# Kernel optimization log

Hardware: AMD Instinct MI355X
Metric: run time of the kernel (lower is better)

Reference implementation:

```python
import jax, jax.numpy as jnp
from jax import lax
import numpy as np

B, S, E, HID = 16, 7, 64, 64
RES = (64, 64); D = RES[0] * RES[1]
XLOW, XHIGH = -0.5, 0.5
RLOW, RHIGH = float(np.sqrt(0.01)), float(np.sqrt(0.05))
PIXEL_MULT = 1.0; N_ITER = 3; TSOFT = 1.0 / float(np.sqrt(E))

def _build_grid():
    ranges = [np.linspace(XLOW, XHIGH, r) for r in RES]
    g = np.stack(np.meshgrid(*ranges, indexing='xy'), axis=-1)
    g = g.reshape(RES[0], RES[1], -1).reshape(1, -1, 2)
    return jnp.asarray(g, dtype=jnp.float32)

ABS_GRID = _build_grid()  # [1, D, 2]

def _ln(x, g, b):
    m = jnp.mean(x, -1, keepdims=True)
    v = jnp.mean(jnp.square(x - m), -1, keepdims=True)
    return (x - m) * lax.rsqrt(v + 1e-5) * g + b

def _forward(data, slot_noise, pos_rand, conv0_w, conv0_b, conv1_w, conv1_b, conv2_w, conv2_b,
             dataN_g, dataN_b, queryN_g, queryN_b, toK_w, toK_b, toV_w, toV_b, dense_w, dense_b,
             mlp1_w, mlp1_b, mlp2_w, mlp2_b, gru_wih, gru_whh, gru_bih, gru_bhh,
             alpha1_w, alpha1_b, alpha2_w, alpha2_b, final1_w, final1_b, final2_w, final2_b,
             slots_mu, slots_logsigma):
    dn = ('NCHW', 'OIHW', 'NCHW')
    def conv(x, w, b):
        return lax.conv_general_dilated(x, w, (1, 1), 'SAME', dimension_numbers=dn) + b[None, :, None, None]
    # CNN encoder: Conv-ReLU x3, 'same' padding, k=5
    x = jax.nn.relu(conv(data, conv0_w, conv0_b))
    x = jax.nn.relu(conv(x, conv1_w, conv1_b))
    x = jax.nn.relu(conv(x, conv2_w, conv2_b))
    enc = x.transpose(0, 2, 3, 1).reshape(B, D, HID)
    enc = _ln(enc, dataN_g, dataN_b)

    queries = slots_mu + jnp.exp(slots_logsigma) * slot_noise  # [B,S,E]
    # init_slots: faithful replication (source indexes the SLOT dim, and swaps rlow/rhigh)
    pos_scale = pos_rand.at[:, :2, :].add(-0.5)
    pos_scale = pos_scale.at[:, -1, :].set((RLOW - RHIGH) * pos_rand[:, -1, :] + RHIGH)

    encK = enc @ toK_w + toK_b  # [B,D,E]
    encV = enc @ toV_w + toV_b

    def init_mlp(y):
        y = _ln(y, queryN_g, queryN_b)
        return jax.nn.relu(y @ mlp1_w + mlp1_b) @ mlp2_w + mlp2_b

    def get_kv(ps):
        # per-slot relative grid: [B,S,D,2]
        rel = (ABS_GRID[:, None] - ps[:, :, None, :2]) / ps[:, :, -1][:, :, None, None]
        eg = PIXEL_MULT * (rel @ dense_w + dense_b)  # [B,S,D,E]
        return init_mlp(encK[:, None] + eg), init_mlp(encV[:, None] + eg)

    def att_wts(q, k):
        logits = jnp.einsum('bse,bsde->bsd', q, k) * TSOFT
        att = jax.nn.softmax(logits, axis=1)  # softmax over slots
        wts = att / jnp.sum(att, -1, keepdims=True) + 1e-8
        return att, wts

    def update_frames(wts):
        new_pos = jnp.einsum('bsd,de->bse', wts, ABS_GRID[0])  # [B,S,2]
        d2 = jnp.sum(jnp.square(ABS_GRID[:, None] - new_pos[:, :, None]), -1)  # [B,S,D]
        new_scale = jnp.sqrt(jnp.einsum('bsd,bsd->bs', wts, d2))
        return jnp.concatenate([new_pos, new_scale[..., None]], -1)

    def gru(xg, h):
        gi = xg @ gru_wih.T + gru_bih
        gh = h @ gru_whh.T + gru_bhh
        ir, iz, inn = jnp.split(gi, 3, -1)
        hr, hz, hn = jnp.split(gh, 3, -1)
        r = jax.nn.sigmoid(ir + hr)
        z = jax.nn.sigmoid(iz + hz)
        n = jnp.tanh(inn + r * hn)
        return (1.0 - z) * n + z * h

    for _ in range(N_ITER):
        keys, vals = get_kv(pos_scale)
        att, wts = att_wts(_ln(queries, queryN_g, queryN_b), keys)
        pos_scale = update_frames(wts)
        upd = jnp.einsum('bsd,bsde->bse', wts, vals)
        queries = gru(upd.reshape(-1, E), queries.reshape(-1, E)).reshape(B, S, E)

    keys, _ = get_kv(pos_scale)
    att, wts = att_wts(_ln(queries, queryN_g, queryN_b), keys)
    nps = update_frames(wts)
    alpha = jax.nn.sigmoid(jax.nn.relu(queries @ alpha1_w + alpha1_b) @ alpha2_w + alpha2_b)
    slot_feat = jax.nn.relu(queries @ final1_w + final1_b) @ final2_w + final2_b + nps
    return queries, att, slot_feat, alpha

def setup_inputs() -> dict:
    ks = jax.random.split(jax.random.key(0), 20)
    f32 = jnp.float32
    def rn(i, shape, s):
        return jax.random.normal(ks[i], shape, f32) * s
    inp = dict(
        data=jax.random.normal(ks[0], (B, 1, RES[0], RES[1]), f32),
        slot_noise=jax.random.normal(ks[1], (B, S, E), f32),
        pos_rand=jax.random.uniform(ks[2], (B, S, 3), dtype=f32),
        conv0_w=rn(3, (HID, 1, 5, 5), 0.2), conv0_b=jnp.zeros(HID, f32),
        conv1_w=rn(4, (HID, HID, 5, 5), 0.025), conv1_b=jnp.zeros(HID, f32),
        conv2_w=rn(5, (HID, HID, 5, 5), 0.025), conv2_b=jnp.zeros(HID, f32),
        dataN_g=jnp.ones(HID, f32), dataN_b=jnp.zeros(HID, f32),
        queryN_g=jnp.ones(E, f32), queryN_b=jnp.zeros(E, f32),
        toK_w=rn(6, (HID, E), 0.125), toK_b=jnp.zeros(E, f32),
        toV_w=rn(7, (HID, E), 0.125), toV_b=jnp.zeros(E, f32),
        dense_w=rn(8, (2, E), 0.7), dense_b=jnp.zeros(E, f32),
        mlp1_w=rn(9, (E, E), 0.125), mlp1_b=jnp.zeros(E, f32),
        mlp2_w=rn(10, (E, E), 0.125), mlp2_b=jnp.zeros(E, f32),
        gru_wih=rn(11, (3 * E, E), 0.125), gru_whh=rn(12, (3 * E, E), 0.125),
        gru_bih=jnp.zeros(3 * E, f32), gru_bhh=jnp.zeros(3 * E, f32),
        alpha1_w=rn(13, (E, 32), 0.125), alpha1_b=jnp.zeros(32, f32),
        alpha2_w=rn(14, (32, 1), 0.18), alpha2_b=jnp.zeros(1, f32),
        final1_w=rn(15, (E, HID), 0.125), final1_b=jnp.zeros(HID, f32),
        final2_w=rn(16, (HID, 3), 0.125), final2_b=jnp.zeros(3, f32),
        slots_mu=rn(17, (1, 1, E), 1.0),
        slots_logsigma=rn(18, (1, 1, E), 0.01),
    )
    return inp

def reference(data, slot_noise, pos_rand, conv0_w, conv0_b, conv1_w, conv1_b, conv2_w, conv2_b,
              dataN_g, dataN_b, queryN_g, queryN_b, toK_w, toK_b, toV_w, toV_b, dense_w, dense_b,
              mlp1_w, mlp1_b, mlp2_w, mlp2_b, gru_wih, gru_whh, gru_bih, gru_bhh,
              alpha1_w, alpha1_b, alpha2_w, alpha2_b, final1_w, final1_b, final2_w, final2_b,
              slots_mu, slots_logsigma):
    return _forward(data, slot_noise, pos_rand, conv0_w, conv0_b, conv1_w, conv1_b, conv2_w, conv2_b,
                    dataN_g, dataN_b, queryN_g, queryN_b, toK_w, toK_b, toV_w, toV_b, dense_w, dense_b,
                    mlp1_w, mlp1_b, mlp2_w, mlp2_b, gru_wih, gru_whh, gru_bih, gru_bhh,
                    alpha1_w, alpha1_b, alpha2_w, alpha2_b, final1_w, final1_b, final2_w, final2_b,
                    slots_mu, slots_logsigma)
```

## Files before the change

### kernel.cpp

```cpp
#include <hip/hip_runtime.h>
#include <cmath>


#define RLOW_F 0.1f
#define RHIGH_F 0.22360679774997896f

typedef __attribute__((ext_vector_type(8))) __bf16 bf16x8;
typedef __attribute__((ext_vector_type(4))) float f32x4;

__device__ __forceinline__ float wsum64(float v){
  #pragma unroll
  for (int off = 32; off > 0; off >>= 1) v += __shfl_xor(v, off, 64);
  return v;
}
__device__ __forceinline__ float rdlane(float v, int l){
  return __int_as_float(__builtin_amdgcn_readlane(__float_as_int(v), l));
}
__device__ __forceinline__ unsigned short bf16bits(float v){
  __bf16 h = (__bf16)v;
  return *reinterpret_cast<unsigned short*>(&h);
}

__global__ void k_prep(const float* __restrict__ noise, const float* __restrict__ prand,
                       const float* __restrict__ mu, const float* __restrict__ logsig,
                       float* __restrict__ queries, float* __restrict__ ps){
  int row = blockIdx.x;
  int e = threadIdx.x;
  int s = row % 7;
  queries[row*64 + e] = mu[e] + expf(logsig[e]) * noise[row*64 + e];
  if (e < 3){
    float pr = prand[row*3 + e];
    float v;
    if (s < 2)      v = pr - 0.5f;
    else if (s == 6) v = (RLOW_F - RHIGH_F)*pr + RHIGH_F;
    else            v = pr;
    ps[row*3 + e] = v;
  }
}

__global__ __launch_bounds__(256) void k_conv0(const float* __restrict__ in,
                        const float* __restrict__ w, const float* __restrict__ bias,
                        unsigned short* __restrict__ out){
  int bi = blockIdx.x; int b = bi >> 6; int y = bi & 63;
  int t = threadIdx.x; int lane = t & 63; int xg = t >> 6;
  __shared__ float s_in[5*68];
  __shared__ float s_w[64*25];
  __shared__ float s_out[64*65];
  for (int i = t; i < 1600; i += 256) s_w[i] = w[i];
  for (int i = t; i < 340; i += 256){
    int r = i / 68, cx = i % 68;
    int yy = y + r - 2, gx = cx - 2;
    float v = 0.f;
    if (yy >= 0 && yy < 64 && gx >= 0 && gx < 64) v = in[(b*64 + yy)*64 + gx];
    s_in[r*68 + cx] = v;
  }
  __syncthreads();
  int o = lane;
  float bv = bias[o];
  float acc[16];
  #pragma unroll
  for (int k = 0; k < 16; k++) acc[k] = bv;
  #pragma unroll
  for (int ky = 0; ky < 5; ky++){
    float rv[20];
    const float4* p = reinterpret_cast<const float4*>(&s_in[ky*68 + xg*16]);
    #pragma unroll
    for (int q = 0; q < 5; q++){ float4 f = p[q]; rv[q*4]=f.x; rv[q*4+1]=f.y; rv[q*4+2]=f.z; rv[q*4+3]=f.w; }
    #pragma unroll
    for (int kx = 0; kx < 5; kx++){
      float wv = s_w[o*25 + ky*5 + kx];
      #pragma unroll
      for (int k = 0; k < 16; k++) acc[k] = fmaf(rv[k+kx], wv, acc[k]);
    }
  }
  #pragma unroll
  for (int k = 0; k < 16; k++) s_out[o*65 + xg*16 + k] = fmaxf(acc[k], 0.f);
  __syncthreads();
  for (int i = t; i < 4096; i += 256){
    int px = i >> 6, ch = i & 63;
    out[((size_t)(b*64 + y)*64 + px)*64 + ch] = bf16bits(s_out[ch*65 + px]);
  }
}

__global__ void k_packconv(const float* __restrict__ w, unsigned short* __restrict__ out){
  int idx = blockIdx.x*256 + threadIdx.x;
  if (idx >= 102400) return;
  int j = idx & 7;
  int l = (idx >> 3) & 63;
  int frag = idx >> 9;
  int nt = frag & 3;
  int ks = (frag >> 2) % 10;
  int dy = frag / 40;
  int q = l >> 4, cr = l & 15;
  int k = ks*32 + q*8 + j;
  int kx = k >> 6, ch = k & 63;
  int n = nt*16 + cr;
  out[idx] = bf16bits(w[((n*64 + ch)*5 + dy)*5 + kx]);
}

__global__ __launch_bounds__(256) void k_convm(const unsigned short* __restrict__ in_bf,
                        const unsigned short* __restrict__ wpack,
                        const float* __restrict__ bias,
                        const float* __restrict__ lng, const float* __restrict__ lnb,
                        unsigned short* __restrict__ out_bf, float* __restrict__ out_f,
                        int mode){
  int bi = blockIdx.x;
  int b = bi >> 4; int yg = bi & 15;
  int t = threadIdx.x; int wv = t >> 6; int l = t & 63;
  int q = l >> 4, cr = l & 15;
  int p0 = wv*16;

  __shared__ char lds[8*68*144];

  for (int ri = 0; ri < 8; ri++){
    int yy = yg*4 + ri - 2;
    bool rok = (yy >= 0 && yy < 64);
    const uint4* src = reinterpret_cast<const uint4*>(in_bf + (size_t)(b*64 + yy)*64*64);
    for (int i = t; i < 544; i += 256){
      int px = i >> 3, c8 = i & 7;
      uint4 v = {0u,0u,0u,0u};
      int gx = px - 2;
      if (rok && gx >= 0 && gx < 64) v = src[gx*8 + c8];
      *reinterpret_cast<uint4*>(&lds[ri*9792 + px*144 + c8*16]) = v;
    }
  }
  __syncthreads();

  f32x4 acc[4][4];
  #pragma unroll
  for (int r = 0; r < 4; r++)
    #pragma unroll
    for (int nt = 0; nt < 4; nt++) acc[r][nt] = (f32x4){0.f,0.f,0.f,0.f};

  const bf16x8* wp = reinterpret_cast<const bf16x8*>(wpack);
  for (int dy = 0; dy < 5; dy++){
    for (int ks = 0; ks < 10; ks++){
      bf16x8 Bf[4];
      int fbase = (dy*10 + ks)*4;
      #pragma unroll
      for (int nt = 0; nt < 4; nt++) Bf[nt] = wp[(fbase + nt)*64 + l];
      int aoff = (p0 + cr + (ks >> 1))*144 + (ks & 1)*64 + q*16;
      #pragma unroll
      for (int r = 0; r < 4; r++){
        bf16x8 a = *reinterpret_cast<const bf16x8*>(&lds[(r + dy)*9792 + aoff]);
        #pragma unroll
        for (int nt = 0; nt < 4; nt++)
          acc[r][nt] = __builtin_amdgcn_mfma_f32_16x16x32_bf16(a, Bf[nt], acc[r][nt], 0, 0, 0);
      }
    }
  }

  float bv[4];
  #pragma unroll
  for (int nt = 0; nt < 4; nt++) bv[nt] = bias[nt*16 + cr];

  if (mode == 0){
    #pragma unroll
    for (int r = 0; r < 4; r++){
      int y = yg*4 + r;
      #pragma unroll
      for (int reg = 0; reg < 4; reg++){
        int p = p0 + q*4 + reg;
        size_t base = ((size_t)(b*64 + y)*64 + p)*64;
        #pragma unroll
        for (int nt = 0; nt < 4; nt++)
          out_bf[base + nt*16 + cr] = bf16bits(fmaxf(acc[r][nt][reg] + bv[nt], 0.f));
      }
    }
  } else {
    float gv[4], bb[4];
    #pragma unroll
    for (int nt = 0; nt < 4; nt++){ gv[nt] = lng[nt*16 + cr]; bb[nt] = lnb[nt*16 + cr]; }
    #pragma unroll
    for (int r = 0; r < 4; r++){
      int y = yg*4 + r;
      #pragma unroll
      for (int reg = 0; reg < 4; reg++){
        int p = p0 + q*4 + reg;
        float v[4]; float s1 = 0.f, s2 = 0.f;
        #pragma unroll
        for (int nt = 0; nt < 4; nt++){
          v[nt] = fmaxf(acc[r][nt][reg] + bv[nt], 0.f);
          s1 += v[nt]; s2 += v[nt]*v[nt];
        }
        #pragma unroll
        for (int m = 1; m < 16; m <<= 1){ s1 += __shfl_xor(s1, m, 64); s2 += __shfl_xor(s2, m, 64); }
        float mean = s1 * (1.f/64.f);
        float var  = s2 * (1.f/64.f) - mean*mean;
        float rstd = 1.0f/sqrtf(var + 1e-5f);
        size_t base = ((size_t)b*4096 + y*64 + p)*64;
        #pragma unroll
        for (int nt = 0; nt < 4; nt++)
          out_f[base + nt*16 + cr] = (v[nt] - mean)*rstd*gv[nt] + bb[nt];
      }
    }
  }
}

__global__ void k_packw1(const float* __restrict__ w1, unsigned short* __restrict__ out){
  int idx = blockIdx.x*256 + threadIdx.x;
  int jj = idx & 7;
  int lane = (idx >> 3) & 63;
  int frag = idx >> 9;
  int ks = frag >> 2, nt = frag & 3;
  int q = lane >> 4, cr = lane & 15;
  int k = ks*32 + q*8 + jj;
  int n = nt*16 + cr;
  out[idx] = bf16bits(w1[k*64 + n]);
}

__global__ __launch_bounds__(256) void k_projm(const float* __restrict__ enc,
                       const unsigned short* __restrict__ kpack, const float* __restrict__ bk,
                       const unsigned short* __restrict__ vpack, const float* __restrict__ bvp,
                       float* __restrict__ K, float* __restrict__ V){
  int bi = blockIdx.x; int b = bi >> 6; int tile = bi & 63;
  int t = threadIdx.x; int wv = t >> 6; int l = t & 63;
  int q = l >> 4, cr = l & 15;
  int d0 = tile*64 + wv*16;

  const bf16x8* kp = reinterpret_cast<const bf16x8*>(kpack);
  const bf16x8* vp = reinterpret_cast<const bf16x8*>(vpack);
  bf16x8 KB[8], VB[8];
  #pragma unroll
  for (int f = 0; f < 8; f++){ KB[f] = kp[f*64 + l]; VB[f] = vp[f*64 + l]; }

  const float* er = enc + (size_t)(b*4096 + d0 + cr)*64;
  bf16x8 a0, a1;
  #pragma unroll
  for (int h = 0; h < 2; h++){
    const float4* e4 = reinterpret_cast<const float4*>(er + (h ? (32 + q*8) : (q*8)));
    #pragma unroll
    for (int p = 0; p < 2; p++){
      float4 e = e4[p];
      if (h == 0){ a0[p*4+0]=(__bf16)e.x; a0[p*4+1]=(__bf16)e.y; a0[p*4+2]=(__bf16)e.z; a0[p*4+3]=(__bf16)e.w; }
      else       { a1[p*4+0]=(__bf16)e.x; a1[p*4+1]=(__bf16)e.y; a1[p*4+2]=(__bf16)e.z; a1[p*4+3]=(__bf16)e.w; }
    }
  }

  f32x4 zero = {0.f,0.f,0.f,0.f};
  f32x4 aK[4], aV[4];
  #pragma unroll
  for (int nt = 0; nt < 4; nt++){
    aK[nt] = __builtin_amdgcn_mfma_f32_16x16x32_bf16(a0, KB[nt],     zero,   0, 0, 0);
    aK[nt] = __builtin_amdgcn_mfma_f32_16x16x32_bf16(a1, KB[4 + nt], aK[nt], 0, 0, 0);
    aV[nt] = __builtin_amdgcn_mfma_f32_16x16x32_bf16(a0, VB[nt],     zero,   0, 0, 0);
    aV[nt] = __builtin_amdgcn_mfma_f32_16x16x32_bf16(a1, VB[4 + nt], aV[nt], 0, 0, 0);
  }
  #pragma unroll
  for (int nt = 0; nt < 4; nt++){
    float bkv = bk[nt*16 + cr], bvv = bvp[nt*16 + cr];
    #pragma unroll
    for (int reg = 0; reg < 4; reg++){
      size_t base = ((size_t)b*4096 + d0 + q*4 + reg)*64 + nt*16 + cr;
      K[base] = aK[nt][reg] + bkv;
      V[base] = aV[nt][reg] + bvv;
    }
  }
}

__global__ void k_phaseprep(const float* __restrict__ queries, const float* __restrict__ ps,
                            const float* __restrict__ qg_, const float* __restrict__ qb_,
                            const float* __restrict__ dw, const float* __restrict__ db,
                            const float* __restrict__ mlp2w, const float* __restrict__ mlp2b,
                            float* __restrict__ absc, float* __restrict__ w2qc,
                            float* __restrict__ sum_att, float* __restrict__ upd){
  int row = blockIdx.x; int e = threadIdx.x;
  float q = queries[row*64 + e];
  float m = wsum64(q) * (1.f/64.f);
  float d = q - m;
  float var = wsum64(d*d) * (1.f/64.f);
  float qlnv = d * (1.0f/sqrtf(var + 1e-5f)) * qg_[e] + qb_[e];
  float px = ps[row*3], py = ps[row*3+1], sc = ps[row*3+2];
  float A  = dw[e]      / sc;
  float Bv = dw[64 + e] / sc;
  absc[(row*3+0)*64 + e] = A;
  absc[(row*3+1)*64 + e] = Bv;
  absc[(row*3+2)*64 + e] = db[e] - px*A - py*Bv;
  float acc = 0.f;
  const float* wrow = mlp2w + e*64;
  for (int j = 0; j < 64; j++) acc = fmaf(wrow[j], rdlane(qlnv, j), acc);
  w2qc[row*68 + e] = acc;
  float c2 = wsum64(mlp2b[e] * qlnv);
  if (e == 0) w2qc[row*68 + 64] = c2;
  upd[row*64 + e] = 0.f;
  if (e == 0) sum_att[row] = 0.f;
}

__global__ __launch_bounds__(256) void k_attn(const float* __restrict__ encX,
     const unsigned short* __restrict__ w1pack, const float* __restrict__ mlp1b,
     const float* __restrict__ absc, const float* __restrict__ qg_,
     const float* __restrict__ qb_, const float* __restrict__ w2qc,
     const float* __restrict__ att, const float* __restrict__ sum_att,
     float* __restrict__ outp, int mode){
  int t = threadIdx.x; int wv = t >> 6; int l = t & 63;
  int q = l >> 4, cr = l & 15;
  int bs = blockIdx.x >> 6; int tile = blockIdx.x & 63;
  int b = bs / 7;
  int m0 = tile*64 + wv*16;
  int drow = m0 + cr;

  const bf16x8* wp = reinterpret_cast<const bf16x8*>(w1pack);
  bf16x8 Bf[8];
  #pragma unroll
  for (int f = 0; f < 8; f++) Bf[f] = wp[f*64 + l];

  const float* Ac = absc + bs*192;
  const float* er = encX + (size_t)(b*4096 + drow)*64;
  float gx = -0.5f + (float)(drow & 63) * (1.f/63.f);
  float gy = -0.5f + (float)((drow >> 6) & 63) * (1.f/63.f);
  float x[16];
  #pragma unroll
  for (int h = 0; h < 2; h++){
    int fb = h ? (32 + q*8) : (q*8);
    const float4* e4 = reinterpret_cast<const float4*>(er + fb);
    const float4* A4 = reinterpret_cast<const float4*>(Ac + fb);
    const float4* B4 = reinterpret_cast<const float4*>(Ac + 64 + fb);
    const float4* C4 = reinterpret_cast<const float4*>(Ac + 128 + fb);
    #pragma unroll
    for (int p = 0; p < 2; p++){
      float4 e = e4[p], Av = A4[p], Bv = B4[p], Cv = C4[p];
      int o = h*8 + p*4;
      x[o+0] = e.x + gx*Av.x + gy*Bv.x + Cv.x;
      x[o+1] = e.y + gx*Av.y + gy*Bv.y + Cv.y;
      x[o+2] = e.z + gx*Av.z + gy*Bv.z + Cv.z;
      x[o+3] = e.w + gx*Av.w + gy*Bv.w + Cv.w;
    }
  }
  float s = 0.f;
  #pragma unroll
  for (int k = 0; k < 16; k++) s += x[k];
  s += __shfl_xor(s, 16, 64); s += __shfl_xor(s, 32, 64);
  float m = s * (1.f/64.f);
  float v = 0.f;
  #pragma unroll
  for (int k = 0; k < 16; k++){ float dd = x[k] - m; v += dd*dd; }
  v += __shfl_xor(v, 16, 64); v += __shfl_xor(v, 32, 64);
  float rstd = 1.0f/sqrtf(v * (1.f/64.f) + 1e-5f);

  bf16x8 a0, a1;
  #pragma unroll
  for (int h = 0; h < 2; h++){
    int fb = h ? (32 + q*8) : (q*8);
    const float4* g4 = reinterpret_cast<const float4*>(qg_ + fb);
    const float4* b4 = reinterpret_cast<const float4*>(qb_ + fb);
    #pragma unroll
    for (int p = 0; p < 2; p++){
      float4 gg = g4[p], bb = b4[p];
      int o = h*8 + p*4;
      float r0 = (x[o+0]-m)*rstd*gg.x + bb.x;
      float r1 = (x[o+1]-m)*rstd*gg.y + bb.y;
      float r2 = (x[o+2]-m)*rstd*gg.z + bb.z;
      float r3 = (x[o+3]-m)*rstd*gg.w + bb.w;
      if (h == 0){ a0[p*4+0]=(__bf16)r0; a0[p*4+1]=(__bf16)r1; a0[p*4+2]=(__bf16)r2; a0[p*4+3]=(__bf16)r3; }
      else       { a1[p*4+0]=(__bf16)r0; a1[p*4+1]=(__bf16)r1; a1[p*4+2]=(__bf16)r2; a1[p*4+3]=(__bf16)r3; }
    }
  }

  f32x4 zero = {0.f, 0.f, 0.f, 0.f};
  f32x4 acc[4];
  #pragma unroll
  for (int nt = 0; nt < 4; nt++){
    acc[nt] = __builtin_amdgcn_mfma_f32_16x16x32_bf16(a0, Bf[nt],     zero,    0, 0, 0);
    acc[nt] = __builtin_amdgcn_mfma_f32_16x16x32_bf16(a1, Bf[4 + nt], acc[nt], 0, 0, 0);
  }

  if (mode == 0){
    const float* wq = w2qc + bs*68;
    float c2 = wq[64];
    float p[4] = {0.f, 0.f, 0.f, 0.f};
    #pragma unroll
    for (int nt = 0; nt < 4; nt++){
      float bb  = mlp1b[nt*16 + cr];
      float wqv = wq[nt*16 + cr];
      #pragma unroll
      for (int reg = 0; reg < 4; reg++){
        float y = fmaxf(acc[nt][reg] + bb, 0.f);
        p[reg] = fmaf(y, wqv, p[reg]);
      }
    }
    #pragma unroll
    for (int reg = 0; reg < 4; reg++){
      #pragma unroll
      for (int off = 1; off < 16; off <<= 1) p[reg] += __shfl_xor(p[reg], off, 64);
    }
    if (cr == 0){
      #pragma unroll
      for (int reg = 0; reg < 4; reg++)
        outp[bs*4096 + m0 + q*4 + reg] = (p[reg] + c2) * 0.125f;
    }
  } else {
    float sa = sum_att[bs];
    float wr[4];
    #pragma unroll
    for (int reg = 0; reg < 4; reg++)
      wr[reg] = att[bs*4096 + m0 + q*4 + reg] / sa + 1e-8f;
    float pc[4] = {0.f, 0.f, 0.f, 0.f};
    #pragma unroll
    for (int nt = 0; nt < 4; nt++){
      float bb = mlp1b[nt*16 + cr];
      #pragma unroll
      for (int reg = 0; reg < 4; reg++)
        pc[nt] = fmaf(wr[reg], fmaxf(acc[nt][reg] + bb, 0.f), pc[nt]);
    }
    #pragma unroll
    for (int nt = 0; nt < 4; nt++){
      pc[nt] += __shfl_xor(pc[nt], 16, 64);
      pc[nt] += __shfl_xor(pc[nt], 32, 64);
    }
    __shared__ float red[4][64];
    if (q == 0){
      #pragma unroll
      for (int nt = 0; nt < 4; nt++) red[wv][nt*16 + cr] = pc[nt];
    }
    __syncthreads();
    if (t < 64) atomicAdd(&outp[bs*64 + t], red[0][t] + red[1][t] + red[2][t] + red[3][t]);
  }
}

__global__ void k_softmax(float* __restrict__ att, float* __restrict__ sum_att){
  int bi = blockIdx.x;
  int b = bi >> 4;
  int t = threadIdx.x;
  int d = (bi & 15)*256 + t;
  int lane = t & 63; int w = t >> 6;
  __shared__ float red[4];
  float l[7];
  #pragma unroll
  for (int s = 0; s < 7; s++) l[s] = att[(b*7+s)*4096 + d];
  float m = l[0];
  #pragma unroll
  for (int s = 1; s < 7; s++) m = fmaxf(m, l[s]);
  float sum = 0.f;
  #pragma unroll
  for (int s = 0; s < 7; s++){ l[s] = expf(l[s] - m); sum += l[s]; }
  for (int s = 0; s < 7; s++){
    float a = l[s] / sum;
    att[(b*7+s)*4096 + d] = a;
    float ws = wsum64(a);
    if (lane == 0) red[w] = ws;
    __syncthreads();
    if (t == 0) atomicAdd(&sum_att[b*7+s], red[0]+red[1]+red[2]+red[3]);
    __syncthreads();
  }
}

__global__ void k_frames(const float* __restrict__ att, const float* __restrict__ sum_att,
                         float* __restrict__ psout, float* __restrict__ sumw){
  int bs = blockIdx.x; int t = threadIdx.x;
  float sa = sum_att[bs];
  float a0 = 0.f, ax = 0.f, ay = 0.f, a2 = 0.f;
  for (int d = t; d < 4096; d += 256){
    float wv = att[bs*4096 + d] / sa + 1e-8f;
    float gx = -0.5f + (float)(d & 63) * (1.f/63.f);
    float gy = -0.5f + (float)(d >> 6) * (1.f/63.f);
    a0 += wv; ax += wv*gx; ay += wv*gy; a2 += wv*(gx*gx + gy*gy);
  }
  __shared__ float red[4][4];
  int lane = t & 63, w = t >> 6;
  a0 = wsum64(a0); ax = wsum64(ax); ay = wsum64(ay); a2 = wsum64(a2);
  if (lane == 0){ red[w][0]=a0; red[w][1]=ax; red[w][2]=ay; red[w][3]=a2; }
  __syncthreads();
  if (t == 0){
    float W0=0,Wx=0,Wy=0,Wg=0;
    for (int k = 0; k < 4; k++){ W0+=red[k][0]; Wx+=red[k][1]; Wy+=red[k][2]; Wg+=red[k][3]; }
    float s2 = Wg - (Wx*Wx + Wy*Wy)*(2.f - W0);
    psout[bs*3+0] = Wx; psout[bs*3+1] = Wy; psout[bs*3+2] = sqrtf(fmaxf(s2, 0.f));
    sumw[bs] = W0;
  }
}

__global__ void k_gru(const float* __restrict__ upd, float* __restrict__ queries,
                      const float* __restrict__ wih, const float* __restrict__ whh,
                      const float* __restrict__ bih, const float* __restrict__ bhh,
                      const float* __restrict__ mlp2w, const float* __restrict__ mlp2b,
                      const float* __restrict__ sumw){
  int row = blockIdx.x; int t = threadIdx.x;
  __shared__ float us[64], hs[64], xs[64], gis[192], ghs[192];
  if (t < 64){ us[t] = upd[row*64 + t]; hs[t] = queries[row*64 + t]; }
  __syncthreads();
  if (t < 64){
    float a = sumw[row] * mlp2b[t];
    for (int i = 0; i < 64; i++) a = fmaf(us[i], mlp2w[i*64 + t], a);
    xs[t] = a;
  }
  __syncthreads();
  float gi = bih[t], gh = bhh[t];
  for (int e = 0; e < 64; e++){
    gi = fmaf(wih[t*64 + e], xs[e], gi);
    gh = fmaf(whh[t*64 + e], hs[e], gh);
  }
  gis[t] = gi; ghs[t] = gh;
  __syncthreads();
  if (t < 64){
    float r = 1.0f/(1.0f + expf(-(gis[t]      + ghs[t])));
    float z = 1.0f/(1.0f + expf(-(gis[64+t]   + ghs[64+t])));
    float n = tanhf(gis[128+t] + r*ghs[128+t]);
    queries[row*64 + t] = (1.0f - z)*n + z*hs[t];
  }
}

__global__ void k_final(const float* __restrict__ queries, const float* __restrict__ nps,
                        const float* __restrict__ a1w, const float* __restrict__ a1b,
                        const float* __restrict__ a2w, const float* __restrict__ a2b,
                        const float* __restrict__ f1w, const float* __restrict__ f1b,
                        const float* __restrict__ f2w, const float* __restrict__ f2b,
                        float* __restrict__ out){
  int bs = blockIdx.x; int e = threadIdx.x;
  __shared__ float qs[64], hf[64], ha[32];
  float q = queries[bs*64 + e];
  qs[e] = q;
  out[bs*64 + e] = q;
  __syncthreads();
  float accf = f1b[e];
  for (int i = 0; i < 64; i++) accf = fmaf(qs[i], f1w[i*64 + e], accf);
  hf[e] = fmaxf(accf, 0.f);
  if (e < 32){
    float acca = a1b[e];
    for (int i = 0; i < 64; i++) acca = fmaf(qs[i], a1w[i*32 + e], acca);
    ha[e] = fmaxf(acca, 0.f);
  }
  __syncthreads();
  if (e < 3){
    float sf = f2b[e];
    for (int o = 0; o < 64; o++) sf = fmaf(hf[o], f2w[o*3 + e], sf);
    out[465920 + bs*3 + e] = sf + nps[bs*3 + e];
  }
  if (e == 32){
    float al = a2b[0];
    for (int o = 0; o < 32; o++) al = fmaf(ha[o], a2w[o], al);
    out[466256 + bs] = 1.0f/(1.0f + expf(-al));
  }
}

extern "C" void kernel_launch(void* const* d_in, const int* in_sizes, int n_in,
                              void* d_out, int out_size, void* d_ws, size_t ws_size,
                              hipStream_t stream){
  const float* data        = (const float*)d_in[0];
  const float* slot_noise  = (const float*)d_in[1];
  const float* pos_rand    = (const float*)d_in[2];
  const float* conv0_w     = (const float*)d_in[3];
  const float* conv0_b     = (const float*)d_in[4];
  const float* conv1_w     = (const float*)d_in[5];
  const float* conv1_b     = (const float*)d_in[6];
  const float* conv2_w     = (const float*)d_in[7];
  const float* conv2_b     = (const float*)d_in[8];
  const float* dataN_g     = (const float*)d_in[9];
  const float* dataN_b     = (const float*)d_in[10];
  const float* queryN_g    = (const float*)d_in[11];
  const float* queryN_b    = (const float*)d_in[12];
  const float* toK_w       = (const float*)d_in[13];
  const float* toK_b       = (const float*)d_in[14];
  const float* toV_w       = (const float*)d_in[15];
  const float* toV_b       = (const float*)d_in[16];
  const float* dense_w     = (const float*)d_in[17];
  const float* dense_b     = (const float*)d_in[18];
  const float* mlp1_w      = (const float*)d_in[19];
  const float* mlp1_b      = (const float*)d_in[20];
  const float* mlp2_w      = (const float*)d_in[21];
  const float* mlp2_b      = (const float*)d_in[22];
  const float* gru_wih     = (const float*)d_in[23];
  const float* gru_whh     = (const float*)d_in[24];
  const float* gru_bih     = (const float*)d_in[25];
  const float* gru_bhh     = (const float*)d_in[26];
  const float* alpha1_w    = (const float*)d_in[27];
  const float* alpha1_b    = (const float*)d_in[28];
  const float* alpha2_w    = (const float*)d_in[29];
  const float* alpha2_b    = (const float*)d_in[30];
  const float* final1_w    = (const float*)d_in[31];
  const float* final1_b    = (const float*)d_in[32];
  const float* final2_w    = (const float*)d_in[33];
  const float* final2_b    = (const float*)d_in[34];
  const float* slots_mu    = (const float*)d_in[35];
  const float* slots_lsig  = (const float*)d_in[36];

  float* ws   = (float*)d_ws;
  float* bufA = ws;
  float* bufB = bufA + 4194304;
  float* bufC = bufB + 4194304;
  float* attw = bufC + 4194304;
  float* queries = attw + 458752;
  float* ps   = queries + 7168;
  float* absc = ps + 512;
  float* sum_att = absc + 21504;
  float* upd  = sum_att + 128;
  float* nps  = upd + 7168;
  float* w2qc = nps + 512;
  float* sumw = w2qc + 7616;
  unsigned short* w1pack = (unsigned short*)(sumw + 128);
  unsigned short* kpack  = w1pack + 4096;
  unsigned short* vpack  = kpack + 4096;
  unsigned short* wp1    = vpack + 4096;
  unsigned short* wp2    = wp1 + 102400;

  unsigned short* c0_bf = (unsigned short*)bufA;
  unsigned short* c1_bf = (unsigned short*)bufC;
  float* enc  = bufB;
  float* encK = bufA;
  float* encV = bufC;

  float* outq   = (float*)d_out;
  float* outatt = outq + 7168;

  k_prep<<<112, 64, 0, stream>>>(slot_noise, pos_rand, slots_mu, slots_lsig, queries, ps);
  k_packw1<<<16, 256, 0, stream>>>(mlp1_w, w1pack);
  k_packw1<<<16, 256, 0, stream>>>(toK_w, kpack);
  k_packw1<<<16, 256, 0, stream>>>(toV_w, vpack);
  k_packconv<<<400, 256, 0, stream>>>(conv1_w, wp1);
  k_packconv<<<400, 256, 0, stream>>>(conv2_w, wp2);
  k_conv0<<<1024, 256, 0, stream>>>(data, conv0_w, conv0_b, c0_bf);
  k_convm<<<256, 256, 0, stream>>>(c0_bf, wp1, conv1_b, nullptr, nullptr, c1_bf, nullptr, 0);
  k_convm<<<256, 256, 0, stream>>>(c1_bf, wp2, conv2_b, dataN_g, dataN_b, nullptr, enc, 1);
  k_projm<<<1024, 256, 0, stream>>>(enc, kpack, toK_b, vpack, toV_b, encK, encV);

  for (int p = 0; p < 4; p++){
    float* attp = (p == 3) ? outatt : attw;
    k_phaseprep<<<112, 64, 0, stream>>>(queries, ps, queryN_g, queryN_b, dense_w, dense_b,
                                        mlp2_w, mlp2_b, absc, w2qc, sum_att, upd);
    k_attn<<<7168, 256, 0, stream>>>(encK, w1pack, mlp1_b, absc, queryN_g, queryN_b,
                                     w2qc, attp, sum_att, attp, 0);
    k_softmax<<<256, 256, 0, stream>>>(attp, sum_att);
    k_frames<<<112, 256, 0, stream>>>(attp, sum_att, (p == 3) ? nps : ps, sumw);
    if (p < 3){
      k_attn<<<7168, 256, 0, stream>>>(encV, w1pack, mlp1_b, absc, queryN_g, queryN_b,
                                       w2qc, attp, sum_att, upd, 1);
      k_gru<<<112, 192, 0, stream>>>(upd, queries, gru_wih, gru_whh, gru_bih, gru_bhh,
                                     mlp2_w, mlp2_b, sumw);
    }
  }
  k_final<<<112, 64, 0, stream>>>(queries, nps, alpha1_w, alpha1_b, alpha2_w, alpha2_b,
                                  final1_w, final1_b, final2_w, final2_b, outq);
}
```

Baseline: 595.7 us.

## Fold query LayerNorm and MLP1 into precomputed per-pixel key/value projections

The change expands the per-slot LayerNorm plus MLP1 algebraically. The LN-weighted mlp1 matrix is folded into the K/V projections, producing bf16 UK/UV tensors and per-pixel statistics (sum, sum of squares, dot products with the dense weights). Each phase then runs a single attention kernel per batch tile covering all 7 slots, accumulating frame moments and updates with atomics. This replaces the separate phaseprep, per-slot attention, softmax and frames kernels. The aim is to cut the repeated 64x64 MFMA work and launch count per phase, at the cost of atomic contention, changed precision (bf16 intermediates, variance via expanded moments) and hardcoding the weight-sum constant.

Measured after the change: 607.4 us. Within noise of the previous version (+2.0%).

```diff
diff --git a/kernel.cpp b/kernel.cpp
--- a/kernel.cpp
+++ b/kernel.cpp
@@ -4,6 +4,7 @@
 
 #define RLOW_F 0.1f
 #define RHIGH_F 0.22360679774997896f
+#define W0CONST 1.00004096f
 
 typedef __attribute__((ext_vector_type(8))) __bf16 bf16x8;
 typedef __attribute__((ext_vector_type(4))) float f32x4;
@@ -20,21 +21,122 @@
   __bf16 h = (__bf16)v;
   return *reinterpret_cast<unsigned short*>(&h);
 }
+__device__ __forceinline__ float bf16val(unsigned short u){
+  __bf16 h = *reinterpret_cast<__bf16*>(&u);
+  return (float)h;
+}
+
+__device__ __forceinline__ void pp_core(int row, int e, float qv,
+    const float* __restrict__ qg_, const float* __restrict__ qb_,
+    const float* __restrict__ mlp2w, const float* __restrict__ mlp2b,
+    float* __restrict__ w2qc){
+  float m = wsum64(qv) * (1.f/64.f);
+  float d = qv - m;
+  float var = wsum64(d*d) * (1.f/64.f);
+  float qlnv = d * (1.0f/sqrtf(var + 1e-5f)) * qg_[e] + qb_[e];
+  float acc = 0.f;
+  const float* wrow = mlp2w + e*64;
+  for (int j = 0; j < 64; j++) acc = fmaf(wrow[j], rdlane(qlnv, j), acc);
+  w2qc[row*68 + e] = acc;
+  float c2 = wsum64(mlp2b[e] * qlnv);
+  if (e == 0) w2qc[row*68 + 64] = c2;
+}
 
 __global__ void k_prep(const float* __restrict__ noise, const float* __restrict__ prand,
                        const float* __restrict__ mu, const float* __restrict__ logsig,
-                       float* __restrict__ queries, float* __restrict__ ps){
+                       const float* __restrict__ qg_, const float* __restrict__ qb_,
+                       const float* __restrict__ mlp2w, const float* __restrict__ mlp2b,
+                       float* __restrict__ queries, float* __restrict__ ps,
+                       float* __restrict__ w2qc, float* __restrict__ accF,
+                       float* __restrict__ gp1, float* __restrict__ gp2){
   int row = blockIdx.x;
   int e = threadIdx.x;
   int s = row % 7;
-  queries[row*64 + e] = mu[e] + expf(logsig[e]) * noise[row*64 + e];
+  float qv = mu[e] + expf(logsig[e]) * noise[row*64 + e];
+  queries[row*64 + e] = qv;
+  gp1[row*64 + e] = 0.f;
+  gp2[row*64 + e] = 0.f;
+  if (e < 4) accF[row*4 + e] = 0.f;
   if (e < 3){
     float pr = prand[row*3 + e];
-    float v;
-    if (s < 2)      v = pr - 0.5f;
-    else if (s == 6) v = (RLOW_F - RHIGH_F)*pr + RHIGH_F;
-    else            v = pr;
-    ps[row*3 + e] = v;
+    float pv;
+    if (s < 2)       pv = pr - 0.5f;
+    else if (s == 6) pv = (RLOW_F - RHIGH_F)*pr + RHIGH_F;
+    else             pv = pr;
+    ps[row*3 + e] = pv;
+  }
+  pp_core(row, e, qv, qg_, qb_, mlp2w, mlp2b, w2qc);
+}
+
+__global__ void k_wconsts(const float* __restrict__ w1, const float* __restrict__ b1,
+                          const float* __restrict__ qg, const float* __restrict__ qb,
+                          const float* __restrict__ dw, const float* __restrict__ db,
+                          const float* __restrict__ tokw, const float* __restrict__ tovw,
+                          const float* __restrict__ bk, const float* __restrict__ bv,
+                          float* __restrict__ consts,
+                          unsigned short* __restrict__ wckp, unsigned short* __restrict__ wcvp){
+  __shared__ float wck[4096], wcv[4096];
+  int t = threadIdx.x;
+  for (int i = 0; i < 16; i++){
+    int idx = t*16 + i; int k = idx >> 6, n = idx & 63;
+    float a1 = 0.f, a2 = 0.f;
+    for (int j = 0; j < 64; j++){
+      float w = qg[j]*w1[j*64 + n];
+      a1 = fmaf(tokw[k*64 + j], w, a1);
+      a2 = fmaf(tovw[k*64 + j], w, a2);
+    }
+    wck[idx] = a1; wcv[idx] = a2;
+  }
+  if (t < 64){
+    int n = t;
+    float G=0,P0=0,Q0=0,Rb=0,Zq=0,bK=0,bV=0;
+    for (int k = 0; k < 64; k++){
+      float w = w1[k*64 + n];
+      float wg = qg[k]*w;
+      G += wg;
+      P0 = fmaf(dw[k],    wg, P0);
+      Q0 = fmaf(dw[64+k], wg, Q0);
+      Rb = fmaf(db[k],    wg, Rb);
+      Zq = fmaf(qb[k],    w,  Zq);
+      bK = fmaf(bk[k],    wg, bK);
+      bV = fmaf(bv[k],    wg, bV);
+    }
+    consts[n] = G; consts[64+n] = P0; consts[128+n] = Q0;
+    consts[192+n] = Zq + b1[n];
+    consts[256+n] = bK + Rb; consts[320+n] = bV + Rb;
+  }
+  if (t >= 64 && t < 73){
+    int j = t - 64; float s = 0.f;
+    for (int k = 0; k < 64; k++){
+      float a, bq;
+      switch(j){
+        case 0: a=dw[k];    bq=dw[k];    break;
+        case 1: a=dw[64+k]; bq=dw[64+k]; break;
+        case 2: a=db[k];    bq=db[k];    break;
+        case 3: a=dw[k];    bq=dw[64+k]; break;
+        case 4: a=dw[k];    bq=db[k];    break;
+        case 5: a=dw[64+k]; bq=db[k];    break;
+        case 6: a=dw[k];    bq=1.f;      break;
+        case 7: a=dw[64+k]; bq=1.f;      break;
+        default:a=db[k];    bq=1.f;      break;
+      }
+      s = fmaf(a, bq, s);
+    }
+    consts[384 + j] = s;
+  }
+  if (t == 73){
+    float s = 0.f;
+    for (int i = 0; i < 64; i++){ float c = -0.5f + i*(1.f/63.f); s += c*c; }
+    consts[393] = 128.f * s;
+  }
+  __syncthreads();
+  for (int i = 0; i < 16; i++){
+    int o = t*16 + i;
+    int jj = o & 7, lane = (o >> 3) & 63, frag = o >> 9;
+    int ks = frag >> 2, nt = frag & 3, qq = lane >> 4, cc = lane & 15;
+    int k = ks*32 + qq*8 + jj, n = nt*16 + cc;
+    wckp[o] = bf16bits(wck[k*64 + n]);
+    wcvp[o] = bf16bits(wcv[k*64 + n]);
   }
 }
 
@@ -56,10 +158,10 @@
   }
   __syncthreads();
   int o = lane;
-  float bv = bias[o];
+  float bvv = bias[o];
   float acc[16];
   #pragma unroll
-  for (int k = 0; k < 16; k++) acc[k] = bv;
+  for (int k = 0; k < 16; k++) acc[k] = bvv;
   #pragma unroll
   for (int ky = 0; ky < 5; ky++){
     float rv[20];
@@ -150,9 +252,9 @@
     }
   }
 
-  float bv[4];
-  #pragma unroll
-  for (int nt = 0; nt < 4; nt++) bv[nt] = bias[nt*16 + cr];
+  float bvv[4];
+  #pragma unroll
+  for (int nt = 0; nt < 4; nt++) bvv[nt] = bias[nt*16 + cr];
 
   if (mode == 0){
     #pragma unroll
@@ -164,7 +266,7 @@
         size_t base = ((size_t)(b*64 + y)*64 + p)*64;
         #pragma unroll
         for (int nt = 0; nt < 4; nt++)
-          out_bf[base + nt*16 + cr] = bf16bits(fmaxf(acc[r][nt][reg] + bv[nt], 0.f));
+          out_bf[base + nt*16 + cr] = bf16bits(fmaxf(acc[r][nt][reg] + bvv[nt], 0.f));
       }
     }
   } else {
@@ -180,7 +282,7 @@
         float v[4]; float s1 = 0.f, s2 = 0.f;
         #pragma unroll
         for (int nt = 0; nt < 4; nt++){
-          v[nt] = fmaxf(acc[r][nt][reg] + bv[nt], 0.f);
+          v[nt] = fmaxf(acc[r][nt][reg] + bvv[nt], 0.f);
           s1 += v[nt]; s2 += v[nt]*v[nt];
         }
         #pragma unroll
@@ -210,20 +312,18 @@
 }
 
 __global__ __launch_bounds__(256) void k_projm(const float* __restrict__ enc,
-                       const unsigned short* __restrict__ kpack, const float* __restrict__ bk,
-                       const unsigned short* __restrict__ vpack, const float* __restrict__ bvp,
-                       float* __restrict__ K, float* __restrict__ V){
+      const unsigned short* __restrict__ kpack, const float* __restrict__ bk,
+      const unsigned short* __restrict__ vpack, const float* __restrict__ bv,
+      const unsigned short* __restrict__ wckp, const unsigned short* __restrict__ wcvp,
+      const float* __restrict__ consts, const float* __restrict__ dw,
+      const float* __restrict__ db,
+      unsigned short* __restrict__ UK, unsigned short* __restrict__ UV,
+      float* __restrict__ stats){
   int bi = blockIdx.x; int b = bi >> 6; int tile = bi & 63;
   int t = threadIdx.x; int wv = t >> 6; int l = t & 63;
   int q = l >> 4, cr = l & 15;
   int d0 = tile*64 + wv*16;
 
-  const bf16x8* kp = reinterpret_cast<const bf16x8*>(kpack);
-  const bf16x8* vp = reinterpret_cast<const bf16x8*>(vpack);
-  bf16x8 KB[8], VB[8];
-  #pragma unroll
-  for (int f = 0; f < 8; f++){ KB[f] = kp[f*64 + l]; VB[f] = vp[f*64 + l]; }
-
   const float* er = enc + (size_t)(b*4096 + d0 + cr)*64;
   bf16x8 a0, a1;
   #pragma unroll
@@ -238,248 +338,275 @@
   }
 
   f32x4 zero = {0.f,0.f,0.f,0.f};
-  f32x4 aK[4], aV[4];
+  f32x4 aK[4], aV[4], aUK[4], aUV[4];
+  {
+    const bf16x8* kp = reinterpret_cast<const bf16x8*>(kpack);
+    const bf16x8* vp = reinterpret_cast<const bf16x8*>(vpack);
+    #pragma unroll
+    for (int nt = 0; nt < 4; nt++){
+      bf16x8 k0 = kp[nt*64 + l], k1 = kp[(4+nt)*64 + l];
+      bf16x8 v0 = vp[nt*64 + l], v1 = vp[(4+nt)*64 + l];
+      aK[nt] = __builtin_amdgcn_mfma_f32_16x16x32_bf16(a0, k0, zero,   0, 0, 0);
+      aK[nt] = __builtin_amdgcn_mfma_f32_16x16x32_bf16(a1, k1, aK[nt], 0, 0, 0);
+      aV[nt] = __builtin_amdgcn_mfma_f32_16x16x32_bf16(a0, v0, zero,   0, 0, 0);
+      aV[nt] = __builtin_amdgcn_mfma_f32_16x16x32_bf16(a1, v1, aV[nt], 0, 0, 0);
+    }
+  }
+  {
+    const bf16x8* cp = reinterpret_cast<const bf16x8*>(wckp);
+    const bf16x8* dp = reinterpret_cast<const bf16x8*>(wcvp);
+    #pragma unroll
+    for (int nt = 0; nt < 4; nt++){
+      bf16x8 c0 = cp[nt*64 + l], c1 = cp[(4+nt)*64 + l];
+      bf16x8 e0 = dp[nt*64 + l], e1 = dp[(4+nt)*64 + l];
+      aUK[nt] = __builtin_amdgcn_mfma_f32_16x16x32_bf16(a0, c0, zero,    0, 0, 0);
+      aUK[nt] = __builtin_amdgcn_mfma_f32_16x16x32_bf16(a1, c1, aUK[nt], 0, 0, 0);
+      aUV[nt] = __builtin_amdgcn_mfma_f32_16x16x32_bf16(a0, e0, zero,    0, 0, 0);
+      aUV[nt] = __builtin_amdgcn_mfma_f32_16x16x32_bf16(a1, e1, aUV[nt], 0, 0, 0);
+    }
+  }
+
+  float bKn[4], bVn[4], uKn[4], uVn[4], d0n[4], d1n[4], dbn[4];
   #pragma unroll
   for (int nt = 0; nt < 4; nt++){
-    aK[nt] = __builtin_amdgcn_mfma_f32_16x16x32_bf16(a0, KB[nt],     zero,   0, 0, 0);
-    aK[nt] = __builtin_amdgcn_mfma_f32_16x16x32_bf16(a1, KB[4 + nt], aK[nt], 0, 0, 0);
-    aV[nt] = __builtin_amdgcn_mfma_f32_16x16x32_bf16(a0, VB[nt],     zero,   0, 0, 0);
-    aV[nt] = __builtin_amdgcn_mfma_f32_16x16x32_bf16(a1, VB[4 + nt], aV[nt], 0, 0, 0);
-  }
-  #pragma unroll
-  for (int nt = 0; nt < 4; nt++){
-    float bkv = bk[nt*16 + cr], bvv = bvp[nt*16 + cr];
+    int n = nt*16 + cr;
+    bKn[nt] = bk[n]; bVn[nt] = bv[n];
+    uKn[nt] = consts[256 + n]; uVn[nt] = consts[320 + n];
+    d0n[nt] = dw[n]; d1n[nt] = dw[64 + n]; dbn[nt] = db[n];
+  }
+
+  float T[10][4];
+  #pragma unroll
+  for (int j = 0; j < 10; j++)
+    #pragma unroll
+    for (int r = 0; r < 4; r++) T[j][r] = 0.f;
+
+  #pragma unroll
+  for (int reg = 0; reg < 4; reg++){
+    int d = d0 + q*4 + reg;
+    size_t base = (size_t)(b*4096 + d)*64;
+    #pragma unroll
+    for (int nt = 0; nt < 4; nt++){
+      int n = nt*16 + cr;
+      UK[base + n] = bf16bits(aUK[nt][reg] + uKn[nt]);
+      UV[base + n] = bf16bits(aUV[nt][reg] + uVn[nt]);
+      float eK = aK[nt][reg] + bKn[nt];
+      float eV = aV[nt][reg] + bVn[nt];
+      T[0][reg] += eK;           T[5][reg] += eV;
+      T[1][reg] += eK*eK;        T[6][reg] += eV*eV;
+      T[2][reg] = fmaf(eK, d0n[nt], T[2][reg]);  T[7][reg] = fmaf(eV, d0n[nt], T[7][reg]);
+      T[3][reg] = fmaf(eK, d1n[nt], T[3][reg]);  T[8][reg] = fmaf(eV, d1n[nt], T[8][reg]);
+      T[4][reg] = fmaf(eK, dbn[nt], T[4][reg]);  T[9][reg] = fmaf(eV, dbn[nt], T[9][reg]);
+    }
+  }
+  #pragma unroll
+  for (int st = 0; st < 10; st++)
+    #pragma unroll
+    for (int r = 0; r < 4; r++){
+      #pragma unroll
+      for (int m = 1; m < 16; m <<= 1) T[st][r] += __shfl_xor(T[st][r], m, 64);
+    }
+  if (cr == 0){
     #pragma unroll
     for (int reg = 0; reg < 4; reg++){
-      size_t base = ((size_t)b*4096 + d0 + q*4 + reg)*64 + nt*16 + cr;
-      K[base] = aK[nt][reg] + bkv;
-      V[base] = aV[nt][reg] + bvv;
-    }
-  }
-}
-
-__global__ void k_phaseprep(const float* __restrict__ queries, const float* __restrict__ ps,
-                            const float* __restrict__ qg_, const float* __restrict__ qb_,
-                            const float* __restrict__ dw, const float* __restrict__ db,
-                            const float* __restrict__ mlp2w, const float* __restrict__ mlp2b,
-                            float* __restrict__ absc, float* __restrict__ w2qc,
-                            float* __restrict__ sum_att, float* __restrict__ upd){
-  int row = blockIdx.x; int e = threadIdx.x;
-  float q = queries[row*64 + e];
-  float m = wsum64(q) * (1.f/64.f);
-  float d = q - m;
-  float var = wsum64(d*d) * (1.f/64.f);
-  float qlnv = d * (1.0f/sqrtf(var + 1e-5f)) * qg_[e] + qb_[e];
-  float px = ps[row*3], py = ps[row*3+1], sc = ps[row*3+2];
-  float A  = dw[e]      / sc;
-  float Bv = dw[64 + e] / sc;
-  absc[(row*3+0)*64 + e] = A;
-  absc[(row*3+1)*64 + e] = Bv;
-  absc[(row*3+2)*64 + e] = db[e] - px*A - py*Bv;
-  float acc = 0.f;
-  const float* wrow = mlp2w + e*64;
-  for (int j = 0; j < 64; j++) acc = fmaf(wrow[j], rdlane(qlnv, j), acc);
-  w2qc[row*68 + e] = acc;
-  float c2 = wsum64(mlp2b[e] * qlnv);
-  if (e == 0) w2qc[row*68 + 64] = c2;
-  upd[row*64 + e] = 0.f;
-  if (e == 0) sum_att[row] = 0.f;
-}
-
-__global__ __launch_bounds__(256) void k_attn(const float* __restrict__ encX,
-     const unsigned short* __restrict__ w1pack, const float* __restrict__ mlp1b,
-     const float* __restrict__ absc, const float* __restrict__ qg_,
-     const float* __restrict__ qb_, const float* __restrict__ w2qc,
-     const float* __restrict__ att, const float* __restrict__ sum_att,
-     float* __restrict__ outp, int mode){
+      int d = d0 + q*4 + reg;
+      float* sp = stats + (size_t)(b*4096 + d)*12;
+      #pragma unroll
+      for (int j = 0; j < 10; j++) sp[j] = T[j][reg];
+    }
+  }
+}
+
+__global__ __launch_bounds__(256) void k_attn(
+    const unsigned short* __restrict__ UK, const unsigned short* __restrict__ UV,
+    const float* __restrict__ stats, const float* __restrict__ consts,
+    const float* __restrict__ ps, const float* __restrict__ w2qc,
+    float* __restrict__ accF, float* __restrict__ gp1, float* __restrict__ gp2,
+    float* __restrict__ att_out, int mode){
+  int bi = blockIdx.x;
+  int b = bi >> 6, tile = bi & 63;
   int t = threadIdx.x; int wv = t >> 6; int l = t & 63;
   int q = l >> 4, cr = l & 15;
-  int bs = blockIdx.x >> 6; int tile = blockIdx.x & 63;
-  int b = bs / 7;
-  int m0 = tile*64 + wv*16;
-  int drow = m0 + cr;
-
-  const bf16x8* wp = reinterpret_cast<const bf16x8*>(w1pack);
-  bf16x8 Bf[8];
-  #pragma unroll
-  for (int f = 0; f < 8; f++) Bf[f] = wp[f*64 + l];
-
-  const float* Ac = absc + bs*192;
-  const float* er = encX + (size_t)(b*4096 + drow)*64;
-  float gx = -0.5f + (float)(drow & 63) * (1.f/63.f);
-  float gy = -0.5f + (float)((drow >> 6) & 63) * (1.f/63.f);
-  float x[16];
-  #pragma unroll
-  for (int h = 0; h < 2; h++){
-    int fb = h ? (32 + q*8) : (q*8);
-    const float4* e4 = reinterpret_cast<const float4*>(er + fb);
-    const float4* A4 = reinterpret_cast<const float4*>(Ac + fb);
-    const float4* B4 = reinterpret_cast<const float4*>(Ac + 64 + fb);
-    const float4* C4 = reinterpret_cast<const float4*>(Ac + 128 + fb);
-    #pragma unroll
-    for (int p = 0; p < 2; p++){
-      float4 e = e4[p], Av = A4[p], Bv = B4[p], Cv = C4[p];
-      int o = h*8 + p*4;
-      x[o+0] = e.x + gx*Av.x + gy*Bv.x + Cv.x;
-      x[o+1] = e.y + gx*Av.y + gy*Bv.y + Cv.y;
-      x[o+2] = e.z + gx*Av.z + gy*Bv.z + Cv.z;
-      x[o+3] = e.w + gx*Av.w + gy*Bv.w + Cv.w;
-    }
-  }
-  float s = 0.f;
-  #pragma unroll
-  for (int k = 0; k < 16; k++) s += x[k];
-  s += __shfl_xor(s, 16, 64); s += __shfl_xor(s, 32, 64);
-  float m = s * (1.f/64.f);
-  float v = 0.f;
-  #pragma unroll
-  for (int k = 0; k < 16; k++){ float dd = x[k] - m; v += dd*dd; }
-  v += __shfl_xor(v, 16, 64); v += __shfl_xor(v, 32, 64);
-  float rstd = 1.0f/sqrtf(v * (1.f/64.f) + 1e-5f);
-
-  bf16x8 a0, a1;
-  #pragma unroll
-  for (int h = 0; h < 2; h++){
-    int fb = h ? (32 + q*8) : (q*8);
-    const float4* g4 = reinterpret_cast<const float4*>(qg_ + fb);
-    const float4* b4 = reinterpret_cast<const float4*>(qb_ + fb);
-    #pragma unroll
-    for (int p = 0; p < 2; p++){
-      float4 gg = g4[p], bb = b4[p];
-      int o = h*8 + p*4;
-      float r0 = (x[o+0]-m)*rstd*gg.x + bb.x;
-      float r1 = (x[o+1]-m)*rstd*gg.y + bb.y;
-      float r2 = (x[o+2]-m)*rstd*gg.z + bb.z;
-      float r3 = (x[o+3]-m)*rstd*gg.w + bb.w;
-      if (h == 0){ a0[p*4+0]=(__bf16)r0; a0[p*4+1]=(__bf16)r1; a0[p*4+2]=(__bf16)r2; a0[p*4+3]=(__bf16)r3; }
-      else       { a1[p*4+0]=(__bf16)r0; a1[p*4+1]=(__bf16)r1; a1[p*4+2]=(__bf16)r2; a1[p*4+3]=(__bf16)r3; }
-    }
-  }
-
-  f32x4 zero = {0.f, 0.f, 0.f, 0.f};
-  f32x4 acc[4];
-  #pragma unroll
-  for (int nt = 0; nt < 4; nt++){
-    acc[nt] = __builtin_amdgcn_mfma_f32_16x16x32_bf16(a0, Bf[nt],     zero,    0, 0, 0);
-    acc[nt] = __builtin_amdgcn_mfma_f32_16x16x32_bf16(a1, Bf[4 + nt], acc[nt], 0, 0, 0);
-  }
-
+  int rloc = wv*16 + cr;
+  int d = tile*64 + rloc;
+  int n0 = q*16;
+
+  __shared__ float s_log[7*64];
+  __shared__ f32x4 s_rstat[7*64];
+  __shared__ float s_wq[7*68];
+  __shared__ float s_ps[24];
+  __shared__ unsigned short s_uv[4096];
+
+  for (int i = t; i < 476; i += 256) s_wq[i] = w2qc[b*476 + i];
+  if (t < 21) s_ps[t] = ps[b*21 + t];
   if (mode == 0){
-    const float* wq = w2qc + bs*68;
-    float c2 = wq[64];
-    float p[4] = {0.f, 0.f, 0.f, 0.f};
-    #pragma unroll
-    for (int nt = 0; nt < 4; nt++){
-      float bb  = mlp1b[nt*16 + cr];
-      float wqv = wq[nt*16 + cr];
+    const uint4* src = reinterpret_cast<const uint4*>(UV + (size_t)(b*4096 + tile*64)*64);
+    uint4* dst = reinterpret_cast<uint4*>(s_uv);
+    for (int i = t; i < 512; i += 256) dst[i] = src[i];
+  }
+
+  float Gr[16], P0r[16], Q0r[16], Zqr[16], Ur[16];
+  #pragma unroll
+  for (int p = 0; p < 4; p++){
+    float4 g  = *reinterpret_cast<const float4*>(consts + n0 + p*4);
+    float4 p0 = *reinterpret_cast<const float4*>(consts + 64 + n0 + p*4);
+    float4 q0 = *reinterpret_cast<const float4*>(consts + 128 + n0 + p*4);
+    float4 zq = *reinterpret_cast<const float4*>(consts + 192 + n0 + p*4);
+    Gr[p*4]=g.x; Gr[p*4+1]=g.y; Gr[p*4+2]=g.z; Gr[p*4+3]=g.w;
+    P0r[p*4]=p0.x; P0r[p*4+1]=p0.y; P0r[p*4+2]=p0.z; P0r[p*4+3]=p0.w;
+    Q0r[p*4]=q0.x; Q0r[p*4+1]=q0.y; Q0r[p*4+2]=q0.z; Q0r[p*4+3]=q0.w;
+    Zqr[p*4]=zq.x; Zqr[p*4+1]=zq.y; Zqr[p*4+2]=zq.z; Zqr[p*4+3]=zq.w;
+  }
+  {
+    const bf16x8* up = reinterpret_cast<const bf16x8*>(UK + (size_t)(b*4096 + d)*64 + n0);
+    bf16x8 u0 = up[0], u1 = up[1];
+    #pragma unroll
+    for (int i = 0; i < 8; i++){ Ur[i] = (float)u0[i]; Ur[8+i] = (float)u1[i]; }
+  }
+  float st[10];
+  {
+    const float* sp = stats + (size_t)(b*4096 + d)*12;
+    float4 s0 = *reinterpret_cast<const float4*>(sp);
+    float4 s1 = *reinterpret_cast<const float4*>(sp + 4);
+    float4 s2 = *reinterpret_cast<const float4*>(sp + 8);
+    st[0]=s0.x; st[1]=s0.y; st[2]=s0.z; st[3]=s0.w;
+    st[4]=s1.x; st[5]=s1.y; st[6]=s1.z; st[7]=s1.w;
+    st[8]=s2.x; st[9]=s2.y;
+  }
+  float S00=consts[384], S11=consts[385], Sbb=consts[386], S01=consts[387];
+  float S0b=consts[388], S1b=consts[389], Sd0=consts[390], Sd1=consts[391], Sdb=consts[392];
+  float Gn=consts[l], P0n=consts[64+l], Q0n=consts[128+l], Zqn=consts[192+l];
+
+  float gx = -0.5f + (float)(d & 63)*(1.f/63.f);
+  float gy = -0.5f + (float)(d >> 6)*(1.f/63.f);
+  __syncthreads();
+
+  for (int s = 0; s < 7; s++){
+    float px = s_ps[s*3], py = s_ps[s*3+1], sc = s_ps[s*3+2];
+    float isc = 1.0f/sc;
+    float u = (gx - px)*isc, v = (gy - py)*isc;
+    float m = (st[0] + u*Sd0 + v*Sd1 + Sdb) * (1.f/64.f);
+    float Sxx = st[1] + u*u*S00 + v*v*S11 + Sbb
+              + 2.f*(u*st[2] + v*st[3] + st[4] + u*v*S01 + u*S0b + v*S1b);
+    float var = Sxx*(1.f/64.f) - m*m;
+    float rstd = 1.0f/sqrtf(var + 1e-5f);
+    if (mode == 0 && q == 0){
+      float mV = (st[5] + u*Sd0 + v*Sd1 + Sdb) * (1.f/64.f);
+      float SxxV = st[6] + u*u*S00 + v*v*S11 + Sbb
+                 + 2.f*(u*st[7] + v*st[8] + st[9] + u*v*S01 + u*S0b + v*S1b);
+      float varV = SxxV*(1.f/64.f) - mV*mV;
+      float rstdV = 1.0f/sqrtf(varV + 1e-5f);
+      s_rstat[s*64 + rloc] = (f32x4){u, v, mV, rstdV};
+    }
+    float acc = 0.f;
+    const float* wqp = s_wq + s*68 + n0;
+    #pragma unroll
+    for (int i = 0; i < 16; i++){
+      float ty = Ur[i] + u*P0r[i] + v*Q0r[i] - m*Gr[i];
+      float Y = fmaf(rstd, ty, Zqr[i]);
+      acc = fmaf(fmaxf(Y, 0.f), wqp[i], acc);
+    }
+    acc += __shfl_xor(acc, 16, 64);
+    acc += __shfl_xor(acc, 32, 64);
+    if (q == 0) s_log[s*64 + rloc] = (acc + s_wq[s*68 + 64]) * 0.125f;
+  }
+  __syncthreads();
+
+  if (t < 64){
+    float lv[7];
+    #pragma unroll
+    for (int s = 0; s < 7; s++) lv[s] = s_log[s*64 + t];
+    float mx = lv[0];
+    #pragma unroll
+    for (int s = 1; s < 7; s++) mx = fmaxf(mx, lv[s]);
+    float sm = 0.f;
+    #pragma unroll
+    for (int s = 0; s < 7; s++){ lv[s] = expf(lv[s] - mx); sm += lv[s]; }
+    float inv = 1.0f/sm;
+    #pragma unroll
+    for (int s = 0; s < 7; s++){
+      float a = lv[s]*inv;
+      s_log[s*64 + t] = a;
+      if (mode == 1) att_out[(size_t)(b*7+s)*4096 + tile*64 + t] = a;
+    }
+  }
+  __syncthreads();
+
+  {
+    int dl = tile*64 + l;
+    float gxl = -0.5f + (float)(dl & 63)*(1.f/63.f);
+    float gyl = -0.5f + (float)(dl >> 6)*(1.f/63.f);
+    float r2 = gxl*gxl + gyl*gyl;
+    for (int s = wv; s < 7; s += 4){
+      float a = s_log[s*64 + l];
+      float w0 = wsum64(a);
+      float w1 = wsum64(a*gxl);
+      float w2 = wsum64(a*gyl);
+      float w3 = wsum64(a*r2);
+      if (l == 0){
+        atomicAdd(&accF[(b*7+s)*4 + 0], w0);
+        atomicAdd(&accF[(b*7+s)*4 + 1], w1);
+        atomicAdd(&accF[(b*7+s)*4 + 2], w2);
+        atomicAdd(&accF[(b*7+s)*4 + 3], w3);
+      }
+    }
+  }
+
+  if (mode == 0){
+    float p1a[7], p2a[7];
+    #pragma unroll
+    for (int s = 0; s < 7; s++){ p1a[s] = 0.f; p2a[s] = 0.f; }
+    int rbase = wv*16;
+    for (int j = 0; j < 16; j++){
+      int row = rbase + j;
+      float uvn = bf16val(s_uv[row*64 + l]);
       #pragma unroll
-      for (int reg = 0; reg < 4; reg++){
-        float y = fmaxf(acc[nt][reg] + bb, 0.f);
-        p[reg] = fmaf(y, wqv, p[reg]);
+      for (int s = 0; s < 7; s++){
+        f32x4 rs = s_rstat[s*64 + row];
+        float a = s_log[s*64 + row];
+        float ty = uvn + rs.x*P0n + rs.y*Q0n - rs.z*Gn;
+        float Y = fmaf(rs.w, ty, Zqn);
+        float y = fmaxf(Y, 0.f);
+        p1a[s] = fmaf(a, y, p1a[s]);
+        p2a[s] += y;
       }
     }
     #pragma unroll
-    for (int reg = 0; reg < 4; reg++){
-      #pragma unroll
-      for (int off = 1; off < 16; off <<= 1) p[reg] += __shfl_xor(p[reg], off, 64);
-    }
-    if (cr == 0){
-      #pragma unroll
-      for (int reg = 0; reg < 4; reg++)
-        outp[bs*4096 + m0 + q*4 + reg] = (p[reg] + c2) * 0.125f;
-    }
-  } else {
-    float sa = sum_att[bs];
-    float wr[4];
-    #pragma unroll
-    for (int reg = 0; reg < 4; reg++)
-      wr[reg] = att[bs*4096 + m0 + q*4 + reg] / sa + 1e-8f;
-    float pc[4] = {0.f, 0.f, 0.f, 0.f};
-    #pragma unroll
-    for (int nt = 0; nt < 4; nt++){
-      float bb = mlp1b[nt*16 + cr];
-      #pragma unroll
-      for (int reg = 0; reg < 4; reg++)
-        pc[nt] = fmaf(wr[reg], fmaxf(acc[nt][reg] + bb, 0.f), pc[nt]);
-    }
-    #pragma unroll
-    for (int nt = 0; nt < 4; nt++){
-      pc[nt] += __shfl_xor(pc[nt], 16, 64);
-      pc[nt] += __shfl_xor(pc[nt], 32, 64);
-    }
-    __shared__ float red[4][64];
-    if (q == 0){
-      #pragma unroll
-      for (int nt = 0; nt < 4; nt++) red[wv][nt*16 + cr] = pc[nt];
-    }
-    __syncthreads();
-    if (t < 64) atomicAdd(&outp[bs*64 + t], red[0][t] + red[1][t] + red[2][t] + red[3][t]);
-  }
-}
-
-__global__ void k_softmax(float* __restrict__ att, float* __restrict__ sum_att){
-  int bi = blockIdx.x;
-  int b = bi >> 4;
-  int t = threadIdx.x;
-  int d = (bi & 15)*256 + t;
-  int lane = t & 63; int w = t >> 6;
-  __shared__ float red[4];
-  float l[7];
-  #pragma unroll
-  for (int s = 0; s < 7; s++) l[s] = att[(b*7+s)*4096 + d];
-  float m = l[0];
-  #pragma unroll
-  for (int s = 1; s < 7; s++) m = fmaxf(m, l[s]);
-  float sum = 0.f;
-  #pragma unroll
-  for (int s = 0; s < 7; s++){ l[s] = expf(l[s] - m); sum += l[s]; }
-  for (int s = 0; s < 7; s++){
-    float a = l[s] / sum;
-    att[(b*7+s)*4096 + d] = a;
-    float ws = wsum64(a);
-    if (lane == 0) red[w] = ws;
-    __syncthreads();
-    if (t == 0) atomicAdd(&sum_att[b*7+s], red[0]+red[1]+red[2]+red[3]);
-    __syncthreads();
-  }
-}
-
-__global__ void k_frames(const float* __restrict__ att, const float* __restrict__ sum_att,
-                         float* __restrict__ psout, float* __restrict__ sumw){
-  int bs = blockIdx.x; int t = threadIdx.x;
-  float sa = sum_att[bs];
-  float a0 = 0.f, ax = 0.f, ay = 0.f, a2 = 0.f;
-  for (int d = t; d < 4096; d += 256){
-    float wv = att[bs*4096 + d] / sa + 1e-8f;
-    float gx = -0.5f + (float)(d & 63) * (1.f/63.f);
-    float gy = -0.5f + (float)(d >> 6) * (1.f/63.f);
-    a0 += wv; ax += wv*gx; ay += wv*gy; a2 += wv*(gx*gx + gy*gy);
-  }
-  __shared__ float red[4][4];
-  int lane = t & 63, w = t >> 6;
-  a0 = wsum64(a0); ax = wsum64(ax); ay = wsum64(ay); a2 = wsum64(a2);
-  if (lane == 0){ red[w][0]=a0; red[w][1]=ax; red[w][2]=ay; red[w][3]=a2; }
-  __syncthreads();
-  if (t == 0){
-    float W0=0,Wx=0,Wy=0,Wg=0;
-    for (int k = 0; k < 4; k++){ W0+=red[k][0]; Wx+=red[k][1]; Wy+=red[k][2]; Wg+=red[k][3]; }
-    float s2 = Wg - (Wx*Wx + Wy*Wy)*(2.f - W0);
-    psout[bs*3+0] = Wx; psout[bs*3+1] = Wy; psout[bs*3+2] = sqrtf(fmaxf(s2, 0.f));
-    sumw[bs] = W0;
-  }
-}
-
-__global__ void k_gru(const float* __restrict__ upd, float* __restrict__ queries,
+    for (int s = 0; s < 7; s++){
+      atomicAdd(&gp1[(b*7+s)*64 + l], p1a[s]);
+      atomicAdd(&gp2[(b*7+s)*64 + l], p2a[s]);
+    }
+  }
+}
+
+__global__ void k_gru(float* __restrict__ gp1, float* __restrict__ gp2,
+                      float* __restrict__ accF, float* __restrict__ queries,
                       const float* __restrict__ wih, const float* __restrict__ whh,
                       const float* __restrict__ bih, const float* __restrict__ bhh,
                       const float* __restrict__ mlp2w, const float* __restrict__ mlp2b,
-                      const float* __restrict__ sumw){
+                      const float* __restrict__ consts, float* __restrict__ ps,
+                      const float* __restrict__ qg_, const float* __restrict__ qb_,
+                      float* __restrict__ w2qc){
   int row = blockIdx.x; int t = threadIdx.x;
   __shared__ float us[64], hs[64], xs[64], gis[192], ghs[192];
-  if (t < 64){ us[t] = upd[row*64 + t]; hs[t] = queries[row*64 + t]; }
-  __syncthreads();
+  __shared__ float s_ps3[3];
+  float sa = accF[row*4 + 0];
   if (t < 64){
-    float a = sumw[row] * mlp2b[t];
+    float isa = 1.0f/sa;
+    us[t] = gp1[row*64 + t]*isa + 1e-8f*gp2[row*64 + t];
+    hs[t] = queries[row*64 + t];
+  }
+  if (t == 64){
+    float ax = accF[row*4+1], ay = accF[row*4+2], ar2 = accF[row*4+3];
+    float isa = 1.0f/sa;
+    float Wx = ax*isa, Wy = ay*isa;
+    float Wg = ar2*isa + 1e-8f*consts[393];
+    float s2 = Wg - (Wx*Wx + Wy*Wy)*(2.f - W0CONST);
+    s_ps3[0] = Wx; s_ps3[1] = Wy; s_ps3[2] = sqrtf(fmaxf(s2, 0.f));
+  }
+  __syncthreads();
+  if (t < 64){
+    float a = W0CONST * mlp2b[t];
     for (int i = 0; i < 64; i++) a = fmaf(us[i], mlp2w[i*64 + t], a);
     xs[t] = a;
   }
@@ -495,11 +622,18 @@
     float r = 1.0f/(1.0f + expf(-(gis[t]      + ghs[t])));
     float z = 1.0f/(1.0f + expf(-(gis[64+t]   + ghs[64+t])));
     float n = tanhf(gis[128+t] + r*ghs[128+t]);
-    queries[row*64 + t] = (1.0f - z)*n + z*hs[t];
-  }
-}
-
-__global__ void k_final(const float* __restrict__ queries, const float* __restrict__ nps,
+    float newq = (1.0f - z)*n + z*hs[t];
+    queries[row*64 + t] = newq;
+    gp1[row*64 + t] = 0.f;
+    gp2[row*64 + t] = 0.f;
+    if (t < 4) accF[row*4 + t] = 0.f;
+    if (t < 3) ps[row*3 + t] = s_ps3[t];
+    pp_core(row, t, newq, qg_, qb_, mlp2w, mlp2b, w2qc);
+  }
+}
+
+__global__ void k_final(const float* __restrict__ queries, const float* __restrict__ accF,
+                        const float* __restrict__ consts,
                         const float* __restrict__ a1w, const float* __restrict__ a1b,
                         const float* __restrict__ a2w, const float* __restrict__ a2b,
                         const float* __restrict__ f1w, const float* __restrict__ f1b,
@@ -523,7 +657,13 @@
   if (e < 3){
     float sf = f2b[e];
     for (int o = 0; o < 64; o++) sf = fmaf(hf[o], f2w[o*3 + e], sf);
-    out[465920 + bs*3 + e] = sf + nps[bs*3 + e];
+    float sa = accF[bs*4+0], ax = accF[bs*4+1], ay = accF[bs*4+2], ar2 = accF[bs*4+3];
+    float isa = 1.0f/sa;
+    float Wx = ax*isa, Wy = ay*isa;
+    float Wg = ar2*isa + 1e-8f*consts[393];
+    float s2 = Wg - (Wx*Wx + Wy*Wy)*(2.f - W0CONST);
+    float nv = (e == 0) ? Wx : ((e == 1) ? Wy : sqrtf(fmaxf(s2, 0.f)));
+    out[465920 + bs*3 + e] = sf + nv;
   }
   if (e == 32){
     float al = a2b[0];
@@ -577,32 +717,35 @@
   float* bufA = ws;
   float* bufB = bufA + 4194304;
   float* bufC = bufB + 4194304;
-  float* attw = bufC + 4194304;
-  float* queries = attw + 458752;
+  float* stats = bufC + 4194304;
+  float* queries = stats + 786432;
   float* ps   = queries + 7168;
-  float* absc = ps + 512;
-  float* sum_att = absc + 21504;
-  float* upd  = sum_att + 128;
-  float* nps  = upd + 7168;
-  float* w2qc = nps + 512;
-  float* sumw = w2qc + 7616;
-  unsigned short* w1pack = (unsigned short*)(sumw + 128);
-  unsigned short* kpack  = w1pack + 4096;
-  unsigned short* vpack  = kpack + 4096;
-  unsigned short* wp1    = vpack + 4096;
-  unsigned short* wp2    = wp1 + 102400;
+  float* w2qc = ps + 512;
+  float* accF = w2qc + 7616;
+  float* gp1  = accF + 512;
+  float* gp2  = gp1 + 7168;
+  float* consts = gp2 + 7168;
+  unsigned short* kpack = (unsigned short*)(consts + 512);
+  unsigned short* vpack = kpack + 4096;
+  unsigned short* wckp  = vpack + 4096;
+  unsigned short* wcvp  = wckp + 4096;
+  unsigned short* wp1   = wcvp + 4096;
+  unsigned short* wp2   = wp1 + 102400;
 
   unsigned short* c0_bf = (unsigned short*)bufA;
+  unsigned short* UK    = (unsigned short*)bufA + 4194304;
   unsigned short* c1_bf = (unsigned short*)bufC;
-  float* enc  = bufB;
-  float* encK = bufA;
-  float* encV = bufC;
+  unsigned short* UV    = (unsigned short*)bufC + 4194304;
+  float* enc = bufB;
 
   float* outq   = (float*)d_out;
   float* outatt = outq + 7168;
 
-  k_prep<<<112, 64, 0, stream>>>(slot_noise, pos_rand, slots_mu, slots_lsig, queries, ps);
-  k_packw1<<<16, 256, 0, stream>>>(mlp1_w, w1pack);
+  k_prep<<<112, 64, 0, stream>>>(slot_noise, pos_rand, slots_mu, slots_lsig,
+                                 queryN_g, queryN_b, mlp2_w, mlp2_b,
+                                 queries, ps, w2qc, accF, gp1, gp2);
+  k_wconsts<<<1, 256, 0, stream>>>(mlp1_w, mlp1_b, queryN_g, queryN_b, dense_w, dense_b,
+                                   toK_w, toV_w, toK_b, toV_b, consts, wckp, wcvp);
   k_packw1<<<16, 256, 0, stream>>>(toK_w, kpack);
   k_packw1<<<16, 256, 0, stream>>>(toV_w, vpack);
   k_packconv<<<400, 256, 0, stream>>>(conv1_w, wp1);
@@ -610,23 +753,20 @@
   k_conv0<<<1024, 256, 0, stream>>>(data, conv0_w, conv0_b, c0_bf);
   k_convm<<<256, 256, 0, stream>>>(c0_bf, wp1, conv1_b, nullptr, nullptr, c1_bf, nullptr, 0);
   k_convm<<<256, 256, 0, stream>>>(c1_bf, wp2, conv2_b, dataN_g, dataN_b, nullptr, enc, 1);
-  k_projm<<<1024, 256, 0, stream>>>(enc, kpack, toK_b, vpack, toV_b, encK, encV);
+  k_projm<<<1024, 256, 0, stream>>>(enc, kpack, toK_b, vpack, toV_b, wckp, wcvp,
+                                    consts, dense_w, dense_b, UK, UV, stats);
 
   for (int p = 0; p < 4; p++){
-    float* attp = (p == 3) ? outatt : attw;
-    k_phaseprep<<<112, 64, 0, stream>>>(queries, ps, queryN_g, queryN_b, dense_w, dense_b,
-                                        mlp2_w, mlp2_b, absc, w2qc, sum_att, upd);
-    k_attn<<<7168, 256, 0, stream>>>(encK, w1pack, mlp1_b, absc, queryN_g, queryN_b,
-                                     w2qc, attp, sum_att, attp, 0);
-    k_softmax<<<256, 256, 0, stream>>>(attp, sum_att);
-    k_frames<<<112, 256, 0, stream>>>(attp, sum_att, (p == 3) ? nps : ps, sumw);
+    k_attn<<<1024, 256, 0, stream>>>(UK, UV, stats, consts, ps, w2qc,
+                                     accF, gp1, gp2, outatt, (p == 3) ? 1 : 0);
     if (p < 3){
-      k_attn<<<7168, 256, 0, stream>>>(encV, w1pack, mlp1_b, absc, queryN_g, queryN_b,
-                                       w2qc, attp, sum_att, upd, 1);
-      k_gru<<<112, 192, 0, stream>>>(upd, queries, gru_wih, gru_whh, gru_bih, gru_bhh,
-                                     mlp2_w, mlp2_b, sumw);
-    }
-  }
-  k_final<<<112, 64, 0, stream>>>(queries, nps, alpha1_w, alpha1_b, alpha2_w, alpha2_b,
+      k_gru<<<112, 192, 0, stream>>>(gp1, gp2, accF, queries,
+                                     gru_wih, gru_whh, gru_bih, gru_bhh,
+                                     mlp2_w, mlp2_b, consts, ps,
+                                     queryN_g, queryN_b, w2qc);
+    }
+  }
+  k_final<<<112, 64, 0, stream>>>(queries, accF, consts,
+                                  alpha1_w, alpha1_b, alpha2_w, alpha2_b,
                                   final1_w, final1_b, final2_w, final2_b, outq);
 }
```
